# Performance work log

Measured on AMD Instinct MI355X. Metric: run time of the kernel, lower is better.

## Reference

```python
import jax, jax.numpy as jnp
import numpy as np

N, IN, H, M, C, E = 200000, 256, 256, 64, 64, 3200000

def gelu(x):
    # torch F.gelu default is exact (erf) gelu
    return jax.nn.gelu(x, approximate=False)

def setup_inputs() -> dict:
    key = jax.random.key(0)
    ks = jax.random.split(key, 12)
    s = 0.02  # small init scale for weights
    p = lambda k, shape: jax.random.normal(k, shape, jnp.float32) * s
    inp = {
        "x": jax.random.normal(ks[0], (N, IN), jnp.float32),
        "edge_index": jax.random.randint(ks[1], (2, E), 0, N),
        "ff1_w0": p(ks[2], (IN, H)),   "ff1_b0": jnp.zeros((H,), jnp.float32),
        "wA0":    p(ks[3], (H, H)),    "wB0":    p(ks[4], (H, M)),
        "ff2_w0": p(ks[5], (2 * H, H)),"ff2_b0": jnp.zeros((H,), jnp.float32),
        "ff1_w1": p(ks[6], (H, H)),    "ff1_b1": jnp.zeros((H,), jnp.float32),
        "wA1":    p(ks[7], (H, H)),    "wB1":    p(ks[8], (H, M)),
        "ff2_w1": p(ks[9], (2 * H, H)),"ff2_b1": jnp.zeros((H,), jnp.float32),
        "head_w": p(ks[10], (H, C)),   "head_b": jnp.zeros((C,), jnp.float32),
    }
    return inp

def _ghm_block(X, ff1_w, ff1_b, wA, wB, ff2_w, ff2_b):
    # FF1
    Hf = gelu(X @ ff1_w + ff1_b)                 # (N, h)
    # HyperAggregation: hypernetwork produces token-mixing weights
    W_tar = gelu(Hf @ wA) @ wB                   # (N, m)
    agg = gelu(Hf.T @ W_tar)                     # (h, m) - mixes over nodes
    agg = (agg @ W_tar.T).T                      # (N, h)
    # root connection: concat aggregated with pre-agg features
    agg = gelu(jnp.concatenate([agg, Hf], axis=1))  # (N, 2h)
    return agg @ ff2_w + ff2_b                   # (N, h)

def reference(x, edge_index, ff1_w0, ff1_b0, wA0, wB0, ff2_w0, ff2_b0,
              ff1_w1, ff1_b1, wA1, wB1, ff2_w1, ff2_b1, head_w, head_b):
    # task='graph', batch=None: whole node set is one fully-connected neighborhood
    X = _ghm_block(x, ff1_w0, ff1_b0, wA0, wB0, ff2_w0, ff2_b0)
    X = _ghm_block(X, ff1_w1, ff1_b1, wA1, wB1, ff2_w1, ff2_b1)
    g = jnp.mean(X, axis=0, keepdims=True)       # (1, h)
    return g @ head_w + head_b                   # (1, C)
```

## Files before the change

### kernel.cpp

```cpp
#include <hip/hip_runtime.h>


typedef unsigned short u16;
typedef unsigned int u32;
typedef short bf16x8 __attribute__((ext_vector_type(8)));
typedef float f32x4 __attribute__((ext_vector_type(4)));

__device__ __forceinline__ float gelu_f(float x) {
  float s = x * x;
  float z = x * fmaf(s, -0.10294348f, -2.3022077f);
  float e = __builtin_amdgcn_exp2f(z);
  return x * __builtin_amdgcn_rcpf(1.0f + e);
}
__device__ __forceinline__ u16 f2b(float f) {
  union { float f; unsigned u; } v; v.f = f;
  unsigned u = v.u;
  u += 0x7fffu + ((u >> 16) & 1u);
  return (u16)(u >> 16);
}

__global__ __launch_bounds__(256) void prep_weights(
    const float* __restrict__ s0, const float* __restrict__ s1,
    const float* __restrict__ s2, const float* __restrict__ s3,
    const float* __restrict__ s4, const float* __restrict__ s5,
    const float* __restrict__ s6, const float* __restrict__ s7,
    u16* __restrict__ dst)
{
  int idx = blockIdx.x * 256 + threadIdx.x;
  if (idx >= 557056) return;
  const float* src; int base, R, C;
  if (idx < 278528) {
    if (idx < 131072) {
      if (idx < 65536) { base = 0;      src = s0; R = 256; C = 256; }
      else             { base = 65536;  src = s1; R = 256; C = 256; }
    } else {
      if (idx < 147456){ base = 131072; src = s2; R = 256; C = 64;  }
      else             { base = 147456; src = s3; R = 512; C = 256; }
    }
  } else {
    int j = idx - 278528;
    if (j < 131072) {
      if (j < 65536)   { base = 278528; src = s4; R = 256; C = 256; }
      else             { base = 344064; src = s5; R = 256; C = 256; }
    } else {
      if (j < 147456)  { base = 409600; src = s6; R = 256; C = 64;  }
      else             { base = 425984; src = s7; R = 512; C = 256; }
    }
  }
  int local = idx - base;
  int o = local / R;
  int k = local - o * R;
  dst[idx] = f2b(src[k * C + o]);
}

template<bool AFP32>
__global__ __launch_bounds__(256, 2) void ff1_hyper(
    const void* __restrict__ Av, const u16* __restrict__ W1T,
    const float* __restrict__ bias, const u16* __restrict__ wAT,
    const u16* __restrict__ wBT, u16* __restrict__ Hf,
    u16* __restrict__ Hfg, u16* __restrict__ Wt, int N)
{
  __shared__ u16 Asm[128][264];
  const int tid = threadIdx.x;
  const int wave = tid >> 6, lane = tid & 63;
  int r0 = blockIdx.x * 128;
  if (r0 > N - 128) r0 = N - 128;

  if constexpr (AFP32) {
    const float* A = (const float*)Av;
    #pragma unroll
    for (int j = 0; j < 32; ++j) {
      int idx = j * 256 + tid;
      int row = idx >> 6, c4 = idx & 63;
      float4 v = *(const float4*)(A + (size_t)(r0 + row) * 256 + c4 * 4);
      uint2 p;
      p.x = (u32)f2b(v.x) | ((u32)f2b(v.y) << 16);
      p.y = (u32)f2b(v.z) | ((u32)f2b(v.w) << 16);
      *(uint2*)&Asm[row][c4 * 4] = p;
    }
  } else {
    const u16* A = (const u16*)Av;
    #pragma unroll
    for (int j = 0; j < 16; ++j) {
      int idx = j * 256 + tid;
      int row = idx >> 5, c8 = idx & 31;
      *(uint4*)&Asm[row][c8 * 8] =
          *(const uint4*)(A + (size_t)(r0 + row) * 256 + c8 * 8);
    }
  }
  __syncthreads();

  const int lm = lane & 15, lq = lane >> 4;
  const int n0 = wave * 64;

  f32x4 acc[8][4] = {};
  #pragma unroll 2
  for (int k0 = 0; k0 < 256; k0 += 32) {
    bf16x8 a[8], b[4];
    #pragma unroll
    for (int ct = 0; ct < 4; ++ct)
      b[ct] = *(const bf16x8*)(W1T + (size_t)(n0 + ct * 16 + lm) * 256 + k0 + lq * 8);
    #pragma unroll
    for (int rt = 0; rt < 8; ++rt)
      a[rt] = *(const bf16x8*)&Asm[rt * 16 + lm][k0 + lq * 8];
    #pragma unroll
    for (int rt = 0; rt < 8; ++rt)
      #pragma unroll
      for (int ct = 0; ct < 4; ++ct)
        acc[rt][ct] = __builtin_amdgcn_mfma_f32_16x16x32_bf16(a[rt], b[ct], acc[rt][ct], 0, 0, 0);
  }
  __syncthreads();
  {
    float bv[4];
    #pragma unroll
    for (int ct = 0; ct < 4; ++ct) bv[ct] = bias[n0 + ct * 16 + lm];
    #pragma unroll
    for (int rt = 0; rt < 8; ++rt)
      #pragma unroll
      for (int ct = 0; ct < 4; ++ct)
        #pragma unroll
        for (int rg = 0; rg < 4; ++rg) {
          float g = gelu_f(acc[rt][ct][rg] + bv[ct]);
          u16 gb = f2b(g);
          int row = rt * 16 + lq * 4 + rg, col = n0 + ct * 16 + lm;
          size_t idx = (size_t)(r0 + row) * 256 + col;
          Hf[idx] = gb;
          Hfg[idx] = f2b(gelu_f(g));
          Asm[row][col] = gb;
        }
  }
  __syncthreads();

  #pragma unroll
  for (int rt = 0; rt < 8; ++rt)
    #pragma unroll
    for (int ct = 0; ct < 4; ++ct)
      acc[rt][ct] = (f32x4){0.f, 0.f, 0.f, 0.f};
  #pragma unroll 2
  for (int k0 = 0; k0 < 256; k0 += 32) {
    bf16x8 a[8], b[4];
    #pragma unroll
    for (int ct = 0; ct < 4; ++ct)
      b[ct] = *(const bf16x8*)(wAT + (size_t)(n0 + ct * 16 + lm) * 256 + k0 + lq * 8);
    #pragma unroll
    for (int rt = 0; rt < 8; ++rt)
      a[rt] = *(const bf16x8*)&Asm[rt * 16 + lm][k0 + lq * 8];
    #pragma unroll
    for (int rt = 0; rt < 8; ++rt)
      #pragma unroll
      for (int ct = 0; ct < 4; ++ct)
        acc[rt][ct] = __builtin_amdgcn_mfma_f32_16x16x32_bf16(a[rt], b[ct], acc[rt][ct], 0, 0, 0);
  }
  __syncthreads();
  #pragma unroll
  for (int rt = 0; rt < 8; ++rt)
    #pragma unroll
    for (int ct = 0; ct < 4; ++ct)
      #pragma unroll
      for (int rg = 0; rg < 4; ++rg)
        Asm[rt * 16 + lq * 4 + rg][n0 + ct * 16 + lm] = f2b(gelu_f(acc[rt][ct][rg]));
  __syncthreads();

  f32x4 acc2[2][4] = {};
  #pragma unroll 2
  for (int k0 = 0; k0 < 256; k0 += 32) {
    bf16x8 a[2], b[4];
    #pragma unroll
    for (int ct = 0; ct < 4; ++ct)
      b[ct] = *(const bf16x8*)(wBT + (size_t)(ct * 16 + lm) * 256 + k0 + lq * 8);
    #pragma unroll
    for (int rt = 0; rt < 2; ++rt)
      a[rt] = *(const bf16x8*)&Asm[wave * 32 + rt * 16 + lm][k0 + lq * 8];
    #pragma unroll
    for (int rt = 0; rt < 2; ++rt)
      #pragma unroll
      for (int ct = 0; ct < 4; ++ct)
        acc2[rt][ct] = __builtin_amdgcn_mfma_f32_16x16x32_bf16(a[rt], b[ct], acc2[rt][ct], 0, 0, 0);
  }
  #pragma unroll
  for (int rt = 0; rt < 2; ++rt)
    #pragma unroll
    for (int ct = 0; ct < 4; ++ct)
      #pragma unroll
      for (int rg = 0; rg < 4; ++rg)
        Wt[(size_t)(r0 + wave * 32 + rt * 16 + lq * 4 + rg) * 64 + ct * 16 + lm] =
            f2b(acc2[rt][ct][rg]);
}

__global__ __launch_bounds__(256) void s_partial(
    const u16* __restrict__ Hf, const u16* __restrict__ Wt,
    float* __restrict__ Spart, int N)
{
  __shared__ u16 HfT[256][72];
  __shared__ u16 WtT[64][72];
  const int tid = threadIdx.x;
  const int wave = tid >> 6, lane = tid & 63;
  const int lm = lane & 15, lq = lane >> 4;
  const int rp = tid & 31;
  const int mb = tid >> 5;
  f32x4 acc[4][4] = {};
  const int nchunk = N >> 6;
  for (int ch = blockIdx.x; ch < nchunk; ch += gridDim.x) {
    const int i0 = ch << 6;
    __syncthreads();
    #pragma unroll
    for (int q = 0; q < 4; ++q) {
      int m = mb + 8 * q;
      const u16* px = Hf + (size_t)(i0 + 2 * rp) * 256 + m * 8;
      uint4 xv = *(const uint4*)px;
      uint4 yv = *(const uint4*)(px + 256);
      u32 xs[4] = {xv.x, xv.y, xv.z, xv.w};
      u32 ys[4] = {yv.x, yv.y, yv.z, yv.w};
      #pragma unroll
      for (int t = 0; t < 4; ++t) {
        *(u32*)&HfT[m * 8 + 2 * t][2 * rp]     = (xs[t] & 0xFFFFu) | (ys[t] << 16);
        *(u32*)&HfT[m * 8 + 2 * t + 1][2 * rp] = (xs[t] >> 16) | (ys[t] & 0xFFFF0000u);
      }
    }
    {
      const u16* px = Wt + (size_t)(i0 + 2 * rp) * 64 + mb * 8;
      uint4 xv = *(const uint4*)px;
      uint4 yv = *(const uint4*)(px + 64);
      u32 xs[4] = {xv.x, xv.y, xv.z, xv.w};
      u32 ys[4] = {yv.x, yv.y, yv.z, yv.w};
      #pragma unroll
      for (int t = 0; t < 4; ++t) {
        *(u32*)&WtT[mb * 8 + 2 * t][2 * rp]     = (xs[t] & 0xFFFFu) | (ys[t] << 16);
        *(u32*)&WtT[mb * 8 + 2 * t + 1][2 * rp] = (xs[t] >> 16) | (ys[t] & 0xFFFF0000u);
      }
    }
    __syncthreads();
    #pragma unroll
    for (int k0 = 0; k0 < 64; k0 += 32) {
      bf16x8 a[4], b[4];
      #pragma unroll
      for (int t = 0; t < 4; ++t)
        a[t] = *(const bf16x8*)&HfT[wave * 64 + t * 16 + lm][k0 + lq * 8];
      #pragma unroll
      for (int m = 0; m < 4; ++m)
        b[m] = *(const bf16x8*)&WtT[m * 16 + lm][k0 + lq * 8];
      #pragma unroll
      for (int t = 0; t < 4; ++t)
        #pragma unroll
        for (int m = 0; m < 4; ++m)
          acc[t][m] = __builtin_amdgcn_mfma_f32_16x16x32_bf16(a[t], b[m], acc[t][m], 0, 0, 0);
    }
  }
  float* out = Spart + (size_t)blockIdx.x * 16384;
  #pragma unroll
  for (int t = 0; t < 4; ++t)
    #pragma unroll
    for (int m = 0; m < 4; ++m)
      #pragma unroll
      for (int rg = 0; rg < 4; ++rg)
        out[(size_t)(wave * 64 + t * 16 + lq * 4 + rg) * 64 + m * 16 + lm] = acc[t][m][rg];
}

__global__ __launch_bounds__(256) void s_reduce(
    const float* __restrict__ Spart, u16* __restrict__ agg, int nparts)
{
  int e = blockIdx.x * 256 + threadIdx.x;
  float s0 = 0.f, s1 = 0.f, s2 = 0.f, s3 = 0.f;
  for (int p = 0; p < nparts; p += 4) {
    s0 += Spart[(size_t)(p + 0) * 16384 + e];
    s1 += Spart[(size_t)(p + 1) * 16384 + e];
    s2 += Spart[(size_t)(p + 2) * 16384 + e];
    s3 += Spart[(size_t)(p + 3) * 16384 + e];
  }
  agg[e] = f2b(gelu_f((s0 + s1) + (s2 + s3)));
}

template<bool COLSUM>
__global__ __launch_bounds__(256, 4) void fused_p_ff2_v5(
    const u16* __restrict__ Wt, const u16* __restrict__ agg,
    const u16* __restrict__ Hfg, const u16* __restrict__ W2T,
    const float* __restrict__ bias, u16* __restrict__ X,
    float* __restrict__ colsum, int N)
{
  __shared__ u16 Pl[64][264];
  const int tid = threadIdx.x;
  const int wave = tid >> 6, lane = tid & 63;
  const int lm = lane & 15, lq = lane >> 4;
  const int r0 = blockIdx.x * 64;
  const int n0 = wave * 64;

  {
    f32x4 acc[4][4] = {};
    #pragma unroll
    for (int k0 = 0; k0 < 64; k0 += 32) {
      bf16x8 a[4], b[4];
      #pragma unroll
      for (int ct = 0; ct < 4; ++ct)
        b[ct] = *(const bf16x8*)(agg + (size_t)(n0 + ct * 16 + lm) * 64 + k0 + lq * 8);
      #pragma unroll
      for (int rt = 0; rt < 4; ++rt)
        a[rt] = *(const bf16x8*)(Wt + (size_t)(r0 + rt * 16 + lm) * 64 + k0 + lq * 8);
      #pragma unroll
      for (int rt = 0; rt < 4; ++rt)
        #pragma unroll
        for (int ct = 0; ct < 4; ++ct)
          acc[rt][ct] = __builtin_amdgcn_mfma_f32_16x16x32_bf16(a[rt], b[ct], acc[rt][ct], 0, 0, 0);
    }
    #pragma unroll
    for (int rt = 0; rt < 4; ++rt)
      #pragma unroll
      for (int ct = 0; ct < 4; ++ct)
        #pragma unroll
        for (int rg = 0; rg < 4; ++rg)
          Pl[rt * 16 + lq * 4 + rg][n0 + ct * 16 + lm] = f2b(gelu_f(acc[rt][ct][rg]));
  }
  __syncthreads();

  f32x4 acc[4][4] = {};
  #pragma unroll 2
  for (int k0 = 0; k0 < 256; k0 += 32) {
    bf16x8 a[4], b[4];
    #pragma unroll
    for (int ct = 0; ct < 4; ++ct)
      b[ct] = *(const bf16x8*)(W2T + (size_t)(n0 + ct * 16 + lm) * 512 + k0 + lq * 8);
    #pragma unroll
    for (int rt = 0; rt < 4; ++rt)
      a[rt] = *(const bf16x8*)&Pl[rt * 16 + lm][k0 + lq * 8];
    #pragma unroll
    for (int rt = 0; rt < 4; ++rt)
      #pragma unroll
      for (int ct = 0; ct < 4; ++ct)
        acc[rt][ct] = __builtin_amdgcn_mfma_f32_16x16x32_bf16(a[rt], b[ct], acc[rt][ct], 0, 0, 0);
  }
  #pragma unroll 2
  for (int k0 = 256; k0 < 512; k0 += 32) {
    bf16x8 a[4], b[4];
    #pragma unroll
    for (int ct = 0; ct < 4; ++ct)
      b[ct] = *(const bf16x8*)(W2T + (size_t)(n0 + ct * 16 + lm) * 512 + k0 + lq * 8);
    #pragma unroll
    for (int rt = 0; rt < 4; ++rt)
      a[rt] = *(const bf16x8*)(Hfg + (size_t)(r0 + rt * 16 + lm) * 256 + (k0 - 256) + lq * 8);
    #pragma unroll
    for (int rt = 0; rt < 4; ++rt)
      #pragma unroll
      for (int ct = 0; ct < 4; ++ct)
        acc[rt][ct] = __builtin_amdgcn_mfma_f32_16x16x32_bf16(a[rt], b[ct], acc[rt][ct], 0, 0, 0);
  }
  float bv[4];
  #pragma unroll
  for (int ct = 0; ct < 4; ++ct) bv[ct] = bias[n0 + ct * 16 + lm];
  if constexpr (!COLSUM) {
    #pragma unroll
    for (int rt = 0; rt < 4; ++rt)
      #pragma unroll
      for (int ct = 0; ct < 4; ++ct)
        #pragma unroll
        for (int rg = 0; rg < 4; ++rg)
          X[(size_t)(r0 + rt * 16 + lq * 4 + rg) * 256 + n0 + ct * 16 + lm] =
              f2b(acc[rt][ct][rg] + bv[ct]);
  } else {
    #pragma unroll
    for (int ct = 0; ct < 4; ++ct) {
      float cs = 0.0f;
      #pragma unroll
      for (int rt = 0; rt < 4; ++rt)
        #pragma unroll
        for (int rg = 0; rg < 4; ++rg) cs += acc[rt][ct][rg] + bv[ct];
      cs += __shfl_down(cs, 32);
      cs += __shfl_down(cs, 16);
      if (lq == 0) atomicAdd(&colsum[n0 + ct * 16 + lm], cs);
    }
  }
}

__global__ __launch_bounds__(64) void head_kernel(
    const float* __restrict__ colsum, const float* __restrict__ head_w,
    const float* __restrict__ head_b, float* __restrict__ out, float invN)
{
  const int c = threadIdx.x;
  float s = head_b[c];
  for (int h = 0; h < 256; ++h) s = fmaf(colsum[h] * invN, head_w[h * 64 + c], s);
  out[c] = s;
}

extern "C" void kernel_launch(void* const* d_in, const int* in_sizes, int n_in,
                              void* d_out, int out_size, void* d_ws, size_t ws_size,
                              hipStream_t stream)
{
  const float* x        = (const float*)d_in[0];
  const float* ff1_w[2] = {(const float*)d_in[2],  (const float*)d_in[8]};
  const float* ff1_b[2] = {(const float*)d_in[3],  (const float*)d_in[9]};
  const float* wA[2]    = {(const float*)d_in[4],  (const float*)d_in[10]};
  const float* wB[2]    = {(const float*)d_in[5],  (const float*)d_in[11]};
  const float* ff2_w[2] = {(const float*)d_in[6],  (const float*)d_in[12]};
  const float* ff2_b[2] = {(const float*)d_in[7],  (const float*)d_in[13]};
  const float* head_w   = (const float*)d_in[14];
  const float* head_b   = (const float*)d_in[15];
  const int N = in_sizes[0] / 256;

  char* ws = (char*)d_ws;
  u16* WT = (u16*)ws;
  u16* W1T[2] = {WT + 0,      WT + 278528};
  u16* wAT[2] = {WT + 65536,  WT + 344064};
  u16* wBT[2] = {WT + 131072, WT + 409600};
  u16* W2T[2] = {WT + 147456, WT + 425984};
  size_t o = 1114112;
  u16* Hf  = (u16*)(ws + o); o += (size_t)N * 256 * 2;
  u16* Hfg = (u16*)(ws + o); o += (size_t)N * 256 * 2;
  u16* TX  = (u16*)(ws + o); o += (size_t)N * 256 * 2;
  u16* Wt  = (u16*)(ws + o); o += (size_t)N * 64 * 2;
  float* Spart  = (float*)(ws + o); o += (size_t)512 * 16384 * 4;
  u16*   agg    = (u16*)(ws + o);   o += 16384 * 2;
  float* colsum = (float*)(ws + o); o += 256 * 4;
  (void)ws_size; (void)n_in; (void)out_size;

  hipMemsetAsync(colsum, 0, 256 * sizeof(float), stream);
  prep_weights<<<2176, 256, 0, stream>>>(ff1_w[0], wA[0], wB[0], ff2_w[0],
                                         ff1_w[1], wA[1], wB[1], ff2_w[1], WT);
  const int G128 = (N + 127) / 128;
  const int G64  = N / 64;
  ff1_hyper<true><<<G128, 256, 0, stream>>>(x, W1T[0], ff1_b[0], wAT[0], wBT[0], Hf, Hfg, Wt, N);
  s_partial<<<512, 256, 0, stream>>>(Hf, Wt, Spart, N);
  s_reduce<<<64, 256, 0, stream>>>(Spart, agg, 512);
  fused_p_ff2_v5<false><<<G64, 256, 0, stream>>>(Wt, agg, Hfg, W2T[0], ff2_b[0], TX, nullptr, N);
  ff1_hyper<false><<<G128, 256, 0, stream>>>(TX, W1T[1], ff1_b[1], wAT[1], wBT[1], Hf, Hfg, Wt, N);
  s_partial<<<512, 256, 0, stream>>>(Hf, Wt, Spart, N);
  s_reduce<<<64, 256, 0, stream>>>(Spart, agg, 512);
  fused_p_ff2_v5<true><<<G64, 256, 0, stream>>>(Wt, agg, Hfg, W2T[1], ff2_b[1], nullptr, colsum, N);
  head_kernel<<<1, 64, 0, stream>>>(colsum, head_w, head_b, (float*)d_out, 1.0f / (float)N);
}
```

Measured before the change: 1.178 ms.

## Software-pipeline weight and tile loads across ff1_hyper, s_partial and ff2 kernels

Adds register double-buffering of the weight-fragment loads in the three ff1_hyper GEMM loops, and register prefetching of the next chunk in s_partial so global loads overlap the MFMA work. The ff2 kernel now stages the Hfg tile into XOR-swizzled LDS with global_load_lds, swizzles the Pl buffer, and runs a single 16-step double-buffered K loop over both halves. This uses more LDS and registers, and the ff2 launch bound drops from 4 to 2 blocks per SM, which may lower occupancy.

```diff
diff --git a/kernel.cpp b/kernel.cpp
--- a/kernel.cpp
+++ b/kernel.cpp
@@ -17,6 +17,9 @@
   unsigned u = v.u;
   u += 0x7fffu + ((u >> 16) & 1u);
   return (u16)(u >> 16);
+}
+__device__ __forceinline__ int swz(int row, int col) {
+  return row * 256 + (((col >> 3) ^ (row & 7)) << 3) + (col & 7);
 }
 
 __global__ __launch_bounds__(256) void prep_weights(
@@ -94,20 +97,28 @@
   const int n0 = wave * 64;
 
   f32x4 acc[8][4] = {};
-  #pragma unroll 2
-  for (int k0 = 0; k0 < 256; k0 += 32) {
-    bf16x8 a[8], b[4];
-    #pragma unroll
-    for (int ct = 0; ct < 4; ++ct)
-      b[ct] = *(const bf16x8*)(W1T + (size_t)(n0 + ct * 16 + lm) * 256 + k0 + lq * 8);
-    #pragma unroll
-    for (int rt = 0; rt < 8; ++rt)
-      a[rt] = *(const bf16x8*)&Asm[rt * 16 + lm][k0 + lq * 8];
-    #pragma unroll
-    for (int rt = 0; rt < 8; ++rt)
-      #pragma unroll
-      for (int ct = 0; ct < 4; ++ct)
-        acc[rt][ct] = __builtin_amdgcn_mfma_f32_16x16x32_bf16(a[rt], b[ct], acc[rt][ct], 0, 0, 0);
+  {
+    bf16x8 bb[2][4];
+    #pragma unroll
+    for (int ct = 0; ct < 4; ++ct)
+      bb[0][ct] = *(const bf16x8*)(W1T + (size_t)(n0 + ct * 16 + lm) * 256 + lq * 8);
+    #pragma unroll
+    for (int s = 0; s < 8; ++s) {
+      const int cur = s & 1;
+      if (s < 7)
+        #pragma unroll
+        for (int ct = 0; ct < 4; ++ct)
+          bb[cur ^ 1][ct] = *(const bf16x8*)(W1T + (size_t)(n0 + ct * 16 + lm) * 256 + (s + 1) * 32 + lq * 8);
+      bf16x8 a[8];
+      #pragma unroll
+      for (int rt = 0; rt < 8; ++rt)
+        a[rt] = *(const bf16x8*)&Asm[rt * 16 + lm][s * 32 + lq * 8];
+      #pragma unroll
+      for (int rt = 0; rt < 8; ++rt)
+        #pragma unroll
+        for (int ct = 0; ct < 4; ++ct)
+          acc[rt][ct] = __builtin_amdgcn_mfma_f32_16x16x32_bf16(a[rt], bb[cur][ct], acc[rt][ct], 0, 0, 0);
+    }
   }
   __syncthreads();
   {
@@ -136,20 +147,28 @@
     #pragma unroll
     for (int ct = 0; ct < 4; ++ct)
       acc[rt][ct] = (f32x4){0.f, 0.f, 0.f, 0.f};
-  #pragma unroll 2
-  for (int k0 = 0; k0 < 256; k0 += 32) {
-    bf16x8 a[8], b[4];
-    #pragma unroll
-    for (int ct = 0; ct < 4; ++ct)
-      b[ct] = *(const bf16x8*)(wAT + (size_t)(n0 + ct * 16 + lm) * 256 + k0 + lq * 8);
-    #pragma unroll
-    for (int rt = 0; rt < 8; ++rt)
-      a[rt] = *(const bf16x8*)&Asm[rt * 16 + lm][k0 + lq * 8];
-    #pragma unroll
-    for (int rt = 0; rt < 8; ++rt)
-      #pragma unroll
-      for (int ct = 0; ct < 4; ++ct)
-        acc[rt][ct] = __builtin_amdgcn_mfma_f32_16x16x32_bf16(a[rt], b[ct], acc[rt][ct], 0, 0, 0);
+  {
+    bf16x8 bb[2][4];
+    #pragma unroll
+    for (int ct = 0; ct < 4; ++ct)
+      bb[0][ct] = *(const bf16x8*)(wAT + (size_t)(n0 + ct * 16 + lm) * 256 + lq * 8);
+    #pragma unroll
+    for (int s = 0; s < 8; ++s) {
+      const int cur = s & 1;
+      if (s < 7)
+        #pragma unroll
+        for (int ct = 0; ct < 4; ++ct)
+          bb[cur ^ 1][ct] = *(const bf16x8*)(wAT + (size_t)(n0 + ct * 16 + lm) * 256 + (s + 1) * 32 + lq * 8);
+      bf16x8 a[8];
+      #pragma unroll
+      for (int rt = 0; rt < 8; ++rt)
+        a[rt] = *(const bf16x8*)&Asm[rt * 16 + lm][s * 32 + lq * 8];
+      #pragma unroll
+      for (int rt = 0; rt < 8; ++rt)
+        #pragma unroll
+        for (int ct = 0; ct < 4; ++ct)
+          acc[rt][ct] = __builtin_amdgcn_mfma_f32_16x16x32_bf16(a[rt], bb[cur][ct], acc[rt][ct], 0, 0, 0);
+    }
   }
   __syncthreads();
   #pragma unroll
@@ -162,20 +181,28 @@
   __syncthreads();
 
   f32x4 acc2[2][4] = {};
-  #pragma unroll 2
-  for (int k0 = 0; k0 < 256; k0 += 32) {
-    bf16x8 a[2], b[4];
-    #pragma unroll
-    for (int ct = 0; ct < 4; ++ct)
-      b[ct] = *(const bf16x8*)(wBT + (size_t)(ct * 16 + lm) * 256 + k0 + lq * 8);
-    #pragma unroll
-    for (int rt = 0; rt < 2; ++rt)
-      a[rt] = *(const bf16x8*)&Asm[wave * 32 + rt * 16 + lm][k0 + lq * 8];
-    #pragma unroll
-    for (int rt = 0; rt < 2; ++rt)
-      #pragma unroll
-      for (int ct = 0; ct < 4; ++ct)
-        acc2[rt][ct] = __builtin_amdgcn_mfma_f32_16x16x32_bf16(a[rt], b[ct], acc2[rt][ct], 0, 0, 0);
+  {
+    bf16x8 bb[2][4];
+    #pragma unroll
+    for (int ct = 0; ct < 4; ++ct)
+      bb[0][ct] = *(const bf16x8*)(wBT + (size_t)(ct * 16 + lm) * 256 + lq * 8);
+    #pragma unroll
+    for (int s = 0; s < 8; ++s) {
+      const int cur = s & 1;
+      if (s < 7)
+        #pragma unroll
+        for (int ct = 0; ct < 4; ++ct)
+          bb[cur ^ 1][ct] = *(const bf16x8*)(wBT + (size_t)(ct * 16 + lm) * 256 + (s + 1) * 32 + lq * 8);
+      bf16x8 a[2];
+      #pragma unroll
+      for (int rt = 0; rt < 2; ++rt)
+        a[rt] = *(const bf16x8*)&Asm[wave * 32 + rt * 16 + lm][s * 32 + lq * 8];
+      #pragma unroll
+      for (int rt = 0; rt < 2; ++rt)
+        #pragma unroll
+        for (int ct = 0; ct < 4; ++ct)
+          acc2[rt][ct] = __builtin_amdgcn_mfma_f32_16x16x32_bf16(a[rt], bb[cur][ct], acc2[rt][ct], 0, 0, 0);
+    }
   }
   #pragma unroll
   for (int rt = 0; rt < 2; ++rt)
@@ -187,7 +214,7 @@
             f2b(acc2[rt][ct][rg]);
 }
 
-__global__ __launch_bounds__(256) void s_partial(
+__global__ __launch_bounds__(256) void s_partial_v2(
     const u16* __restrict__ Hf, const u16* __restrict__ Wt,
     float* __restrict__ Spart, int N)
 {
@@ -198,19 +225,30 @@
   const int lm = lane & 15, lq = lane >> 4;
   const int rp = tid & 31;
   const int mb = tid >> 5;
+  uint4 hx[4][2], wx[2];
+  auto issue = [&](int ch) {
+    int i0 = ch << 6;
+    #pragma unroll
+    for (int q = 0; q < 4; ++q) {
+      const u16* px = Hf + (size_t)(i0 + 2 * rp) * 256 + (mb + 8 * q) * 8;
+      hx[q][0] = *(const uint4*)px;
+      hx[q][1] = *(const uint4*)(px + 256);
+    }
+    const u16* pw = Wt + (size_t)(i0 + 2 * rp) * 64 + mb * 8;
+    wx[0] = *(const uint4*)pw;
+    wx[1] = *(const uint4*)(pw + 64);
+  };
   f32x4 acc[4][4] = {};
   const int nchunk = N >> 6;
-  for (int ch = blockIdx.x; ch < nchunk; ch += gridDim.x) {
-    const int i0 = ch << 6;
+  int ch = blockIdx.x;
+  if (ch < nchunk) issue(ch);
+  for (; ch < nchunk; ch += gridDim.x) {
     __syncthreads();
     #pragma unroll
     for (int q = 0; q < 4; ++q) {
       int m = mb + 8 * q;
-      const u16* px = Hf + (size_t)(i0 + 2 * rp) * 256 + m * 8;
-      uint4 xv = *(const uint4*)px;
-      uint4 yv = *(const uint4*)(px + 256);
-      u32 xs[4] = {xv.x, xv.y, xv.z, xv.w};
-      u32 ys[4] = {yv.x, yv.y, yv.z, yv.w};
+      u32 xs[4] = {hx[q][0].x, hx[q][0].y, hx[q][0].z, hx[q][0].w};
+      u32 ys[4] = {hx[q][1].x, hx[q][1].y, hx[q][1].z, hx[q][1].w};
       #pragma unroll
       for (int t = 0; t < 4; ++t) {
         *(u32*)&HfT[m * 8 + 2 * t][2 * rp]     = (xs[t] & 0xFFFFu) | (ys[t] << 16);
@@ -218,11 +256,8 @@
       }
     }
     {
-      const u16* px = Wt + (size_t)(i0 + 2 * rp) * 64 + mb * 8;
-      uint4 xv = *(const uint4*)px;
-      uint4 yv = *(const uint4*)(px + 64);
-      u32 xs[4] = {xv.x, xv.y, xv.z, xv.w};
-      u32 ys[4] = {yv.x, yv.y, yv.z, yv.w};
+      u32 xs[4] = {wx[0].x, wx[0].y, wx[0].z, wx[0].w};
+      u32 ys[4] = {wx[1].x, wx[1].y, wx[1].z, wx[1].w};
       #pragma unroll
       for (int t = 0; t < 4; ++t) {
         *(u32*)&WtT[mb * 8 + 2 * t][2 * rp]     = (xs[t] & 0xFFFFu) | (ys[t] << 16);
@@ -230,6 +265,7 @@
       }
     }
     __syncthreads();
+    if (ch + (int)gridDim.x < nchunk) issue(ch + (int)gridDim.x);
     #pragma unroll
     for (int k0 = 0; k0 < 64; k0 += 32) {
       bf16x8 a[4], b[4];
@@ -271,19 +307,32 @@
 }
 
 template<bool COLSUM>
-__global__ __launch_bounds__(256, 4) void fused_p_ff2_v5(
+__global__ __launch_bounds__(256, 2) void fused_p_ff2_v6(
     const u16* __restrict__ Wt, const u16* __restrict__ agg,
     const u16* __restrict__ Hfg, const u16* __restrict__ W2T,
     const float* __restrict__ bias, u16* __restrict__ X,
     float* __restrict__ colsum, int N)
 {
-  __shared__ u16 Pl[64][264];
+  __shared__ u16 Hsm[64 * 256];
+  __shared__ u16 Pl[64 * 256];
   const int tid = threadIdx.x;
   const int wave = tid >> 6, lane = tid & 63;
   const int lm = lane & 15, lq = lane >> 4;
   const int r0 = blockIdx.x * 64;
   const int n0 = wave * 64;
 
+  #pragma unroll
+  for (int t = 0; t < 8; ++t) {
+    int unit = (wave * 8 + t) * 64 + lane;
+    int row = unit >> 5, ksw = unit & 31;
+    int kc = ksw ^ (row & 7);
+    const u16* g = Hfg + (size_t)(r0 + row) * 256 + kc * 8;
+    __builtin_amdgcn_global_load_lds(
+        (const __attribute__((address_space(1))) void*)g,
+        (__attribute__((address_space(3))) void*)(Hsm + (size_t)(wave * 8 + t) * 512),
+        16, 0, 0);
+  }
+
   {
     f32x4 acc[4][4] = {};
     #pragma unroll
@@ -307,40 +356,37 @@
       for (int ct = 0; ct < 4; ++ct)
         #pragma unroll
         for (int rg = 0; rg < 4; ++rg)
-          Pl[rt * 16 + lq * 4 + rg][n0 + ct * 16 + lm] = f2b(gelu_f(acc[rt][ct][rg]));
-  }
-  __syncthreads();
-
+          Pl[swz(rt * 16 + lq * 4 + rg, n0 + ct * 16 + lm)] = f2b(gelu_f(acc[rt][ct][rg]));
+  }
+  __syncthreads();
+
+  auto ldb = [&](int s, bf16x8* b) {
+    #pragma unroll
+    for (int ct = 0; ct < 4; ++ct)
+      b[ct] = *(const bf16x8*)(W2T + (size_t)(n0 + ct * 16 + lm) * 512 + s * 32 + lq * 8);
+  };
+  auto lda = [&](int s, bf16x8* a) {
+    const u16* base = (s < 8) ? Pl : Hsm;
+    const int k0 = (s & 7) * 32;
+    #pragma unroll
+    for (int rt = 0; rt < 4; ++rt) {
+      int row = rt * 16 + lm;
+      a[rt] = *(const bf16x8*)&base[swz(row, k0 + lq * 8)];
+    }
+  };
   f32x4 acc[4][4] = {};
-  #pragma unroll 2
-  for (int k0 = 0; k0 < 256; k0 += 32) {
-    bf16x8 a[4], b[4];
-    #pragma unroll
-    for (int ct = 0; ct < 4; ++ct)
-      b[ct] = *(const bf16x8*)(W2T + (size_t)(n0 + ct * 16 + lm) * 512 + k0 + lq * 8);
+  bf16x8 ab[2][4], bb[2][4];
+  ldb(0, bb[0]);
+  lda(0, ab[0]);
+  #pragma unroll
+  for (int s = 0; s < 16; ++s) {
+    const int cur = s & 1, nxt = cur ^ 1;
+    if (s < 15) { ldb(s + 1, bb[nxt]); lda(s + 1, ab[nxt]); }
     #pragma unroll
     for (int rt = 0; rt < 4; ++rt)
-      a[rt] = *(const bf16x8*)&Pl[rt * 16 + lm][k0 + lq * 8];
-    #pragma unroll
-    for (int rt = 0; rt < 4; ++rt)
       #pragma unroll
       for (int ct = 0; ct < 4; ++ct)
-        acc[rt][ct] = __builtin_amdgcn_mfma_f32_16x16x32_bf16(a[rt], b[ct], acc[rt][ct], 0, 0, 0);
-  }
-  #pragma unroll 2
-  for (int k0 = 256; k0 < 512; k0 += 32) {
-    bf16x8 a[4], b[4];
-    #pragma unroll
-    for (int ct = 0; ct < 4; ++ct)
-      b[ct] = *(const bf16x8*)(W2T + (size_t)(n0 + ct * 16 + lm) * 512 + k0 + lq * 8);
-    #pragma unroll
-    for (int rt = 0; rt < 4; ++rt)
-      a[rt] = *(const bf16x8*)(Hfg + (size_t)(r0 + rt * 16 + lm) * 256 + (k0 - 256) + lq * 8);
-    #pragma unroll
-    for (int rt = 0; rt < 4; ++rt)
-      #pragma unroll
-      for (int ct = 0; ct < 4; ++ct)
-        acc[rt][ct] = __builtin_amdgcn_mfma_f32_16x16x32_bf16(a[rt], b[ct], acc[rt][ct], 0, 0, 0);
+        acc[rt][ct] = __builtin_amdgcn_mfma_f32_16x16x32_bf16(ab[cur][rt], bb[cur][ct], acc[rt][ct], 0, 0, 0);
   }
   float bv[4];
   #pragma unroll
@@ -416,12 +462,12 @@
   const int G128 = (N + 127) / 128;
   const int G64  = N / 64;
   ff1_hyper<true><<<G128, 256, 0, stream>>>(x, W1T[0], ff1_b[0], wAT[0], wBT[0], Hf, Hfg, Wt, N);
-  s_partial<<<512, 256, 0, stream>>>(Hf, Wt, Spart, N);
+  s_partial_v2<<<512, 256, 0, stream>>>(Hf, Wt, Spart, N);
   s_reduce<<<64, 256, 0, stream>>>(Spart, agg, 512);
-  fused_p_ff2_v5<false><<<G64, 256, 0, stream>>>(Wt, agg, Hfg, W2T[0], ff2_b[0], TX, nullptr, N);
+  fused_p_ff2_v6<false><<<G64, 256, 0, stream>>>(Wt, agg, Hfg, W2T[0], ff2_b[0], TX, nullptr, N);
   ff1_hyper<false><<<G128, 256, 0, stream>>>(TX, W1T[1], ff1_b[1], wAT[1], wBT[1], Hf, Hfg, Wt, N);
-  s_partial<<<512, 256, 0, stream>>>(Hf, Wt, Spart, N);
+  s_partial_v2<<<512, 256, 0, stream>>>(Hf, Wt, Spart, N);
   s_reduce<<<64, 256, 0, stream>>>(Spart, agg, 512);
-  fused_p_ff2_v5<true><<<G64, 256, 0, stream>>>(Wt, agg, Hfg, W2T[1], ff2_b[1], nullptr, colsum, N);
+  fused_p_ff2_v6<true><<<G64, 256, 0, stream>>>(Wt, agg, Hfg, W2T[1], ff2_b[1], nullptr, colsum, N);
   head_kernel<<<1, 64, 0, stream>>>(colsum, head_w, head_b, (float*)d_out, 1.0f / (float)N);
 }
```

Result: faster. 1.077 ms (-8.5%).
